# Performance work log

Measured on AMD Instinct MI355X. Metric: run time of the kernel, lower is better.

The kernel has to match this reference:

```python
import jax, jax.numpy as jnp
import numpy as np

N_NODES = 100000
N_EDGES = 1600000
D_FEAT = 128
NUM_UNITS = 128


def setup_inputs() -> dict:
    key = jax.random.key(0)
    k1, k2, k3, k4, k5 = jax.random.split(key, 5)
    H = jax.random.normal(k1, (N_NODES, D_FEAT), dtype=jnp.float32)
    edge_vals = jax.random.uniform(k2, (N_EDGES,), dtype=jnp.float32)
    W = jax.random.normal(k3, (D_FEAT, NUM_UNITS), dtype=jnp.float32) / np.sqrt(D_FEAT)
    b = jnp.zeros((NUM_UNITS,), dtype=jnp.float32)
    edge_src = jax.random.randint(k4, (N_EDGES,), 0, N_NODES, dtype=jnp.int32)
    edge_dst = jax.random.randint(k5, (N_EDGES,), 0, N_NODES, dtype=jnp.int32)
    return {"H": H, "edge_vals": edge_vals, "W": W, "b": b,
            "edge_src": edge_src, "edge_dst": edge_dst}


def reference(H, edge_vals, W, b, edge_src, edge_dst):
    # SpMM: AH[i] = sum_{e: src[e]==i} val[e] * H[dst[e]]
    gathered = edge_vals[:, None] * H[edge_dst]            # [E, F]
    AH = jax.ops.segment_sum(gathered, edge_src, num_segments=N_NODES)  # [N, F]
    # Dense projection + bias + relu (tf.layers.Dense with tf.nn.relu)
    return jax.nn.relu(AH @ W + b)
```

## Files before the change

kernel.cpp:

```cpp
#include <hip/hip_runtime.h>

#define N_NODES  100000
#define N_EDGES  1600000
#define D        128
#define NBUCK    1563
#define BCAP     1536
#define OCAP     8192
#define FCHUNK   8192

typedef __attribute__((ext_vector_type(8))) short bf16x8;
typedef __attribute__((ext_vector_type(4))) float f32x4;

__device__ __forceinline__ unsigned short f2bf(float x) {
    unsigned u = __float_as_uint(x);
    u += 0x7fffu + ((u >> 16) & 1u);
    return (unsigned short)(u >> 16);
}

__global__ __launch_bounds__(256) void wconvert(
    const float* __restrict__ W, unsigned short* __restrict__ Wfrag)
{
    int t = blockIdx.x * 256 + threadIdx.x;
    if (t >= 128 * 128) return;
    int k = t >> 7, n = t & 127;
    int c = n >> 4, cc = n & 15, ks = k >> 5, g = (k >> 3) & 3, j = k & 7;
    int lane = g * 16 + cc;
    Wfrag[(size_t)(((c * 4 + ks) * 64) + lane) * 8 + j] = f2bf(W[t]);
}

__global__ __launch_bounds__(256) void gemm_mfma(
    const float* __restrict__ H, const unsigned short* __restrict__ Wfrag,
    unsigned short* __restrict__ HWb)
{
    const int wid  = threadIdx.x >> 6;
    const int lane = threadIdx.x & 63;
    const int row16 = blockIdx.x * 64 + wid * 16;
    const int g = lane >> 4;

    int arow = row16 + (lane & 15);
    if (arow >= N_NODES) arow = N_NODES - 1;

    f32x4 acc[8];
#pragma unroll
    for (int c = 0; c < 8; ++c) acc[c] = (f32x4){0.f, 0.f, 0.f, 0.f};

#pragma unroll
    for (int ks = 0; ks < 4; ++ks) {
        const float* ap = H + (size_t)arow * D + ks * 32 + g * 8;
        float4 a0 = *reinterpret_cast<const float4*>(ap);
        float4 a1 = *reinterpret_cast<const float4*>(ap + 4);
        bf16x8 af;
        af[0] = (short)f2bf(a0.x); af[1] = (short)f2bf(a0.y);
        af[2] = (short)f2bf(a0.z); af[3] = (short)f2bf(a0.w);
        af[4] = (short)f2bf(a1.x); af[5] = (short)f2bf(a1.y);
        af[6] = (short)f2bf(a1.z); af[7] = (short)f2bf(a1.w);
#pragma unroll
        for (int c = 0; c < 8; ++c) {
            bf16x8 bf = *reinterpret_cast<const bf16x8*>(
                Wfrag + (size_t)((c * 4 + ks) * 64 + lane) * 8);
            acc[c] = __builtin_amdgcn_mfma_f32_16x16x32_bf16(af, bf, acc[c], 0, 0, 0);
        }
    }

#pragma unroll
    for (int c = 0; c < 8; ++c) {
#pragma unroll
        for (int r = 0; r < 4; ++r) {
            int orow = row16 + g * 4 + r;
            if (orow < N_NODES)
                HWb[(size_t)orow * D + c * 16 + (lane & 15)] = f2bf(acc[c][r]);
        }
    }
}

__global__ __launch_bounds__(256) void fill_bucket(
    const int* __restrict__ src, const int* __restrict__ dst,
    const float* __restrict__ vals, int* __restrict__ ccursor,
    int2* __restrict__ sedge_raw, int4* __restrict__ oflow,
    int* __restrict__ oflow_cnt)
{
    __shared__ int lhist[NBUCK];
    __shared__ int lbase[NBUCK];
    const int t = threadIdx.x;
    for (int i = t; i < NBUCK; i += 256) lhist[i] = 0;
    __syncthreads();
    const int e0 = blockIdx.x * FCHUNK;
    const int e1 = min(e0 + FCHUNK, N_EDGES);
    for (int e = e0 + t; e < e1; e += 256)
        atomicAdd(&lhist[src[e] >> 6], 1);
    __syncthreads();
    for (int i = t; i < NBUCK; i += 256) {
        int c = lhist[i];
        lbase[i] = c ? atomicAdd(&ccursor[i], c) : 0;
        lhist[i] = 0;
    }
    __syncthreads();
    for (int e = e0 + t; e < e1; e += 256) {
        int s = src[e];
        int bkt = s >> 6;
        int pos = lbase[bkt] + atomicAdd(&lhist[bkt], 1);
        if (pos < BCAP) {
            int2 p;
            p.x = dst[e] | ((s & 63) << 17);
            p.y = __float_as_int(vals[e]);
            sedge_raw[(size_t)bkt * BCAP + pos] = p;
        } else {
            int oc = atomicAdd(oflow_cnt, 1);
            if (oc < OCAP) oflow[oc] = make_int4(s, dst[e], __float_as_int(vals[e]), 0);
        }
    }
}

__global__ __launch_bounds__(256) void sort_gather(
    const unsigned short* __restrict__ HWb, const int2* __restrict__ sedge_raw,
    const int* __restrict__ ccursor, const int4* __restrict__ oflow,
    const int* __restrict__ oflow_cnt, const float* __restrict__ bias,
    float* __restrict__ out)
{
    __shared__ int2 eLds[BCAP];
    __shared__ int h[64];
    __shared__ int ex[64];
    __shared__ int cur[64];
    const int bkt = blockIdx.x;
    const int t = threadIdx.x;
    const size_t base = (size_t)bkt * BCAP;
    const int cnt = min(ccursor[bkt], BCAP);

    if (t < 64) h[t] = 0;
    __syncthreads();
    for (int j = t; j < cnt; j += 256)
        atomicAdd(&h[(sedge_raw[base + j].x >> 17) & 63], 1);
    __syncthreads();
    if (t < 64) {
        int v = h[t];
        int x = v;
        for (int off = 1; off < 64; off <<= 1) {
            int y = __shfl_up(x, off);
            if (t >= off) x += y;
        }
        ex[t] = x - v;
        cur[t] = 0;
    }
    __syncthreads();
    for (int j = t; j < cnt; j += 256) {
        int2 e = sedge_raw[base + j];
        int r = (e.x >> 17) & 63;
        int pos = ex[r] + atomicAdd(&cur[r], 1);
        e.x &= 0x1FFFF;
        eLds[pos] = e;
    }
    __syncthreads();

    const int wid = t >> 6, lane = t & 63;
    const int ovc = *oflow_cnt;
    const float2 bv = *reinterpret_cast<const float2*>(bias + lane * 2);
    for (int ln = wid; ln < 64; ln += 4) {
        int node = bkt * 64 + ln;
        if (node >= N_NODES) break;
        const int j0 = ex[ln], j1 = ex[ln] + h[ln];
        float ax = 0.f, ay = 0.f, bx = 0.f, by = 0.f;
        float cx = 0.f, cy = 0.f, dx = 0.f, dy = 0.f;
        int j = j0;
        for (; j + 4 <= j1; j += 4) {
            int2 e0 = eLds[j],     e1 = eLds[j + 1];
            int2 e2 = eLds[j + 2], e3 = eLds[j + 3];
            unsigned u0 = *reinterpret_cast<const unsigned*>(HWb + (size_t)e0.x * D + lane * 2);
            unsigned u1 = *reinterpret_cast<const unsigned*>(HWb + (size_t)e1.x * D + lane * 2);
            unsigned u2 = *reinterpret_cast<const unsigned*>(HWb + (size_t)e2.x * D + lane * 2);
            unsigned u3 = *reinterpret_cast<const unsigned*>(HWb + (size_t)e3.x * D + lane * 2);
            float v0 = __int_as_float(e0.y), v1 = __int_as_float(e1.y);
            float v2 = __int_as_float(e2.y), v3 = __int_as_float(e3.y);
            ax += v0 * __uint_as_float(u0 << 16);
            ay += v0 * __uint_as_float(u0 & 0xffff0000u);
            bx += v1 * __uint_as_float(u1 << 16);
            by += v1 * __uint_as_float(u1 & 0xffff0000u);
            cx += v2 * __uint_as_float(u2 << 16);
            cy += v2 * __uint_as_float(u2 & 0xffff0000u);
            dx += v3 * __uint_as_float(u3 << 16);
            dy += v3 * __uint_as_float(u3 & 0xffff0000u);
        }
        for (; j < j1; ++j) {
            int2 e = eLds[j];
            unsigned u = *reinterpret_cast<const unsigned*>(HWb + (size_t)e.x * D + lane * 2);
            float v = __int_as_float(e.y);
            ax += v * __uint_as_float(u << 16);
            ay += v * __uint_as_float(u & 0xffff0000u);
        }
        for (int q = 0; q < ovc; ++q) {
            int4 e = oflow[q];
            if (e.x == node) {
                unsigned u = *reinterpret_cast<const unsigned*>(HWb + (size_t)e.y * D + lane * 2);
                float v = __int_as_float(e.z);
                ax += v * __uint_as_float(u << 16);
                ay += v * __uint_as_float(u & 0xffff0000u);
            }
        }
        float2 o;
        o.x = fmaxf((ax + bx) + (cx + dx) + bv.x, 0.f);
        o.y = fmaxf((ay + by) + (cy + dy) + bv.y, 0.f);
        *reinterpret_cast<float2*>(out + (size_t)node * D + lane * 2) = o;
    }
}

extern "C" void kernel_launch(void* const* d_in, const int* in_sizes, int n_in,
                              void* d_out, int out_size, void* d_ws, size_t ws_size,
                              hipStream_t stream) {
    const float* H    = (const float*)d_in[0];
    const float* vals = (const float*)d_in[1];
    const float* W    = (const float*)d_in[2];
    const float* b    = (const float*)d_in[3];
    const int*   src  = (const int*)d_in[4];
    const int*   dst  = (const int*)d_in[5];
    float* out = (float*)d_out;

    unsigned short* HWb   = (unsigned short*)d_ws;
    unsigned short* Wfrag = HWb + (size_t)N_NODES * D;
    int2* sedge_raw = (int2*)(Wfrag + 128 * 128);
    int*  ccursor   = (int*)(sedge_raw + (size_t)NBUCK * BCAP);
    int*  oflow_cnt = ccursor + NBUCK;
    int4* oflow     = (int4*)(oflow_cnt + 3);

    hipMemsetAsync(ccursor, 0, (NBUCK + 1) * sizeof(int), stream);

    wconvert<<<64, 256, 0, stream>>>(W, Wfrag);
    gemm_mfma<<<(N_NODES + 63) / 64, 256, 0, stream>>>(H, Wfrag, HWb);
    fill_bucket<<<(N_EDGES + FCHUNK - 1) / FCHUNK, 256, 0, stream>>>(
        src, dst, vals, ccursor, sedge_raw, oflow, oflow_cnt);
    sort_gather<<<NBUCK, 256, 0, stream>>>(HWb, sedge_raw, ccursor, oflow,
                                           oflow_cnt, b, out);
}
```

Before: 134.2 us.

## Fuse weight convert, GEMM and edge bucketing into one launch; halve bucket size

Merges the W-conversion, MFMA projection and edge-bucket fill kernels into one heterogeneous launch. Blocks below GEMM_BLOCKS convert W into LDS and run the GEMM, and the remaining blocks bucket edges, so the two independent phases can run concurrently and two launches disappear. Buckets shrink from 64 to 32 nodes (3125 buckets, capacity 768), and sort_gather keeps its edges in registers instead of reading global memory twice. In exchange, every GEMM block re-reads and converts all of W, and the smaller buckets are more likely to overflow into the serial overflow list.

Measured after the change: 128.1 us. 1.05x faster.

```diff
diff --git a/kernel.cpp b/kernel.cpp
--- a/kernel.cpp
+++ b/kernel.cpp
@@ -3,10 +3,11 @@
 #define N_NODES  100000
 #define N_EDGES  1600000
 #define D        128
-#define NBUCK    1563
-#define BCAP     1536
+#define NBUCK    3125
+#define BCAP     768
 #define OCAP     8192
-#define FCHUNK   8192
+#define FCHUNK   4096
+#define GEMM_BLOCKS 1563
 
 typedef __attribute__((ext_vector_type(8))) short bf16x8;
 typedef __attribute__((ext_vector_type(4))) float f32x4;
@@ -17,96 +18,110 @@
     return (unsigned short)(u >> 16);
 }
 
-__global__ __launch_bounds__(256) void wconvert(
-    const float* __restrict__ W, unsigned short* __restrict__ Wfrag)
+__global__ __launch_bounds__(256) void mega(
+    const float* __restrict__ H, const float* __restrict__ W,
+    const int* __restrict__ src, const int* __restrict__ dst,
+    const float* __restrict__ vals, unsigned short* __restrict__ HWb,
+    int* __restrict__ ccursor, int2* __restrict__ sedge_raw,
+    int4* __restrict__ oflow, int* __restrict__ oflow_cnt)
 {
-    int t = blockIdx.x * 256 + threadIdx.x;
-    if (t >= 128 * 128) return;
-    int k = t >> 7, n = t & 127;
-    int c = n >> 4, cc = n & 15, ks = k >> 5, g = (k >> 3) & 3, j = k & 7;
-    int lane = g * 16 + cc;
-    Wfrag[(size_t)(((c * 4 + ks) * 64) + lane) * 8 + j] = f2bf(W[t]);
-}
-
-__global__ __launch_bounds__(256) void gemm_mfma(
-    const float* __restrict__ H, const unsigned short* __restrict__ Wfrag,
-    unsigned short* __restrict__ HWb)
-{
-    const int wid  = threadIdx.x >> 6;
-    const int lane = threadIdx.x & 63;
-    const int row16 = blockIdx.x * 64 + wid * 16;
-    const int g = lane >> 4;
-
-    int arow = row16 + (lane & 15);
-    if (arow >= N_NODES) arow = N_NODES - 1;
-
-    f32x4 acc[8];
-#pragma unroll
-    for (int c = 0; c < 8; ++c) acc[c] = (f32x4){0.f, 0.f, 0.f, 0.f};
-
-#pragma unroll
-    for (int ks = 0; ks < 4; ++ks) {
-        const float* ap = H + (size_t)arow * D + ks * 32 + g * 8;
-        float4 a0 = *reinterpret_cast<const float4*>(ap);
-        float4 a1 = *reinterpret_cast<const float4*>(ap + 4);
-        bf16x8 af;
-        af[0] = (short)f2bf(a0.x); af[1] = (short)f2bf(a0.y);
-        af[2] = (short)f2bf(a0.z); af[3] = (short)f2bf(a0.w);
-        af[4] = (short)f2bf(a1.x); af[5] = (short)f2bf(a1.y);
-        af[6] = (short)f2bf(a1.z); af[7] = (short)f2bf(a1.w);
+    __shared__ char smem[32768];
+    const int t = threadIdx.x;
+
+    if (blockIdx.x < GEMM_BLOCKS) {
+        short* wlds = (short*)smem;
+        {
+            const int n   = t & 127;
+            const int kb0 = (t >> 7) * 4;
+            const int c = n >> 4, cc = n & 15;
+#pragma unroll
+            for (int q = 0; q < 16; ++q) {
+                int kbase = q * 8 + kb0;
+                float w0 = W[(kbase + 0) * 128 + n];
+                float w1 = W[(kbase + 1) * 128 + n];
+                float w2 = W[(kbase + 2) * 128 + n];
+                float w3 = W[(kbase + 3) * 128 + n];
+                int ks = kbase >> 5, g = (kbase >> 3) & 3, j0 = kbase & 7;
+                short4 pk;
+                pk.x = (short)f2bf(w0);
+                pk.y = (short)f2bf(w1);
+                pk.z = (short)f2bf(w2);
+                pk.w = (short)f2bf(w3);
+                *reinterpret_cast<short4*>(
+                    &wlds[(size_t)(((c * 4 + ks) * 64) + g * 16 + cc) * 8 + j0]) = pk;
+            }
+        }
+        __syncthreads();
+
+        const int wid  = t >> 6;
+        const int lane = t & 63;
+        const int row16 = blockIdx.x * 64 + wid * 16;
+        const int g = lane >> 4;
+
+        int arow = row16 + (lane & 15);
+        if (arow >= N_NODES) arow = N_NODES - 1;
+
+        f32x4 acc[8];
+#pragma unroll
+        for (int c = 0; c < 8; ++c) acc[c] = (f32x4){0.f, 0.f, 0.f, 0.f};
+
+#pragma unroll
+        for (int ks = 0; ks < 4; ++ks) {
+            const float* ap = H + (size_t)arow * D + ks * 32 + g * 8;
+            float4 a0 = *reinterpret_cast<const float4*>(ap);
+            float4 a1 = *reinterpret_cast<const float4*>(ap + 4);
+            bf16x8 af;
+            af[0] = (short)f2bf(a0.x); af[1] = (short)f2bf(a0.y);
+            af[2] = (short)f2bf(a0.z); af[3] = (short)f2bf(a0.w);
+            af[4] = (short)f2bf(a1.x); af[5] = (short)f2bf(a1.y);
+            af[6] = (short)f2bf(a1.z); af[7] = (short)f2bf(a1.w);
+#pragma unroll
+            for (int c = 0; c < 8; ++c) {
+                bf16x8 bf = *reinterpret_cast<const bf16x8*>(
+                    &wlds[(size_t)((c * 4 + ks) * 64 + lane) * 8]);
+                acc[c] = __builtin_amdgcn_mfma_f32_16x16x32_bf16(af, bf, acc[c], 0, 0, 0);
+            }
+        }
+
 #pragma unroll
         for (int c = 0; c < 8; ++c) {
-            bf16x8 bf = *reinterpret_cast<const bf16x8*>(
-                Wfrag + (size_t)((c * 4 + ks) * 64 + lane) * 8);
-            acc[c] = __builtin_amdgcn_mfma_f32_16x16x32_bf16(af, bf, acc[c], 0, 0, 0);
-        }
-    }
-
-#pragma unroll
-    for (int c = 0; c < 8; ++c) {
-#pragma unroll
-        for (int r = 0; r < 4; ++r) {
-            int orow = row16 + g * 4 + r;
-            if (orow < N_NODES)
-                HWb[(size_t)orow * D + c * 16 + (lane & 15)] = f2bf(acc[c][r]);
-        }
-    }
-}
-
-__global__ __launch_bounds__(256) void fill_bucket(
-    const int* __restrict__ src, const int* __restrict__ dst,
-    const float* __restrict__ vals, int* __restrict__ ccursor,
-    int2* __restrict__ sedge_raw, int4* __restrict__ oflow,
-    int* __restrict__ oflow_cnt)
-{
-    __shared__ int lhist[NBUCK];
-    __shared__ int lbase[NBUCK];
-    const int t = threadIdx.x;
-    for (int i = t; i < NBUCK; i += 256) lhist[i] = 0;
-    __syncthreads();
-    const int e0 = blockIdx.x * FCHUNK;
-    const int e1 = min(e0 + FCHUNK, N_EDGES);
-    for (int e = e0 + t; e < e1; e += 256)
-        atomicAdd(&lhist[src[e] >> 6], 1);
-    __syncthreads();
-    for (int i = t; i < NBUCK; i += 256) {
-        int c = lhist[i];
-        lbase[i] = c ? atomicAdd(&ccursor[i], c) : 0;
-        lhist[i] = 0;
-    }
-    __syncthreads();
-    for (int e = e0 + t; e < e1; e += 256) {
-        int s = src[e];
-        int bkt = s >> 6;
-        int pos = lbase[bkt] + atomicAdd(&lhist[bkt], 1);
-        if (pos < BCAP) {
-            int2 p;
-            p.x = dst[e] | ((s & 63) << 17);
-            p.y = __float_as_int(vals[e]);
-            sedge_raw[(size_t)bkt * BCAP + pos] = p;
-        } else {
-            int oc = atomicAdd(oflow_cnt, 1);
-            if (oc < OCAP) oflow[oc] = make_int4(s, dst[e], __float_as_int(vals[e]), 0);
+#pragma unroll
+            for (int r = 0; r < 4; ++r) {
+                int orow = row16 + g * 4 + r;
+                if (orow < N_NODES)
+                    HWb[(size_t)orow * D + c * 16 + (lane & 15)] = f2bf(acc[c][r]);
+            }
+        }
+    } else {
+        int* lhist = (int*)smem;
+        int* lbase = lhist + NBUCK;
+        for (int i = t; i < NBUCK; i += 256) lhist[i] = 0;
+        __syncthreads();
+        const int fb = blockIdx.x - GEMM_BLOCKS;
+        const int e0 = fb * FCHUNK;
+        const int e1 = min(e0 + FCHUNK, N_EDGES);
+        for (int e = e0 + t; e < e1; e += 256)
+            atomicAdd(&lhist[src[e] >> 5], 1);
+        __syncthreads();
+        for (int i = t; i < NBUCK; i += 256) {
+            int c = lhist[i];
+            lbase[i] = c ? atomicAdd(&ccursor[i], c) : 0;
+            lhist[i] = 0;
+        }
+        __syncthreads();
+        for (int e = e0 + t; e < e1; e += 256) {
+            int s = src[e];
+            int bkt = s >> 5;
+            int pos = lbase[bkt] + atomicAdd(&lhist[bkt], 1);
+            if (pos < BCAP) {
+                int2 p;
+                p.x = dst[e] | ((s & 31) << 17);
+                p.y = __float_as_int(vals[e]);
+                sedge_raw[(size_t)bkt * BCAP + pos] = p;
+            } else {
+                int oc = atomicAdd(oflow_cnt, 1);
+                if (oc < OCAP) oflow[oc] = make_int4(s, dst[e], __float_as_int(vals[e]), 0);
+            }
         }
     }
 }
@@ -118,23 +133,33 @@
     float* __restrict__ out)
 {
     __shared__ int2 eLds[BCAP];
-    __shared__ int h[64];
-    __shared__ int ex[64];
-    __shared__ int cur[64];
+    __shared__ int h[32];
+    __shared__ int ex[32];
+    __shared__ int cur[32];
     const int bkt = blockIdx.x;
     const int t = threadIdx.x;
     const size_t base = (size_t)bkt * BCAP;
     const int cnt = min(ccursor[bkt], BCAP);
 
-    if (t < 64) h[t] = 0;
-    __syncthreads();
-    for (int j = t; j < cnt; j += 256)
-        atomicAdd(&h[(sedge_raw[base + j].x >> 17) & 63], 1);
-    __syncthreads();
-    if (t < 64) {
+    if (t < 32) { h[t] = 0; }
+    __syncthreads();
+
+    int2 myE[3]; int myR[3];
+#pragma unroll
+    for (int q = 0; q < 3; ++q) {
+        int j = t + q * 256;
+        myR[q] = -1;
+        if (j < cnt) {
+            myE[q] = sedge_raw[base + j];
+            myR[q] = (myE[q].x >> 17) & 31;
+            atomicAdd(&h[myR[q]], 1);
+        }
+    }
+    __syncthreads();
+    if (t < 32) {
         int v = h[t];
         int x = v;
-        for (int off = 1; off < 64; off <<= 1) {
+        for (int off = 1; off < 32; off <<= 1) {
             int y = __shfl_up(x, off);
             if (t >= off) x += y;
         }
@@ -142,21 +167,23 @@
         cur[t] = 0;
     }
     __syncthreads();
-    for (int j = t; j < cnt; j += 256) {
-        int2 e = sedge_raw[base + j];
-        int r = (e.x >> 17) & 63;
-        int pos = ex[r] + atomicAdd(&cur[r], 1);
-        e.x &= 0x1FFFF;
-        eLds[pos] = e;
+#pragma unroll
+    for (int q = 0; q < 3; ++q) {
+        if (myR[q] >= 0) {
+            int pos = ex[myR[q]] + atomicAdd(&cur[myR[q]], 1);
+            int2 e;
+            e.x = myE[q].x & 0x1FFFF;
+            e.y = myE[q].y;
+            eLds[pos] = e;
+        }
     }
     __syncthreads();
 
     const int wid = t >> 6, lane = t & 63;
     const int ovc = *oflow_cnt;
     const float2 bv = *reinterpret_cast<const float2*>(bias + lane * 2);
-    for (int ln = wid; ln < 64; ln += 4) {
-        int node = bkt * 64 + ln;
-        if (node >= N_NODES) break;
+    for (int ln = wid; ln < 32; ln += 4) {
+        int node = bkt * 32 + ln;
         const int j0 = ex[ln], j1 = ex[ln] + h[ln];
         float ax = 0.f, ay = 0.f, bx = 0.f, by = 0.f;
         float cx = 0.f, cy = 0.f, dx = 0.f, dy = 0.f;
@@ -213,19 +240,17 @@
     const int*   dst  = (const int*)d_in[5];
     float* out = (float*)d_out;
 
-    unsigned short* HWb   = (unsigned short*)d_ws;
-    unsigned short* Wfrag = HWb + (size_t)N_NODES * D;
-    int2* sedge_raw = (int2*)(Wfrag + 128 * 128);
+    unsigned short* HWb = (unsigned short*)d_ws;
+    int2* sedge_raw = (int2*)(HWb + (size_t)N_NODES * D);
     int*  ccursor   = (int*)(sedge_raw + (size_t)NBUCK * BCAP);
     int*  oflow_cnt = ccursor + NBUCK;
     int4* oflow     = (int4*)(oflow_cnt + 3);
 
     hipMemsetAsync(ccursor, 0, (NBUCK + 1) * sizeof(int), stream);
 
-    wconvert<<<64, 256, 0, stream>>>(W, Wfrag);
-    gemm_mfma<<<(N_NODES + 63) / 64, 256, 0, stream>>>(H, Wfrag, HWb);
-    fill_bucket<<<(N_EDGES + FCHUNK - 1) / FCHUNK, 256, 0, stream>>>(
-        src, dst, vals, ccursor, sedge_raw, oflow, oflow_cnt);
+    const int FILL_BLOCKS = (N_EDGES + FCHUNK - 1) / FCHUNK;
+    mega<<<GEMM_BLOCKS + FILL_BLOCKS, 256, 0, stream>>>(
+        H, W, src, dst, vals, HWb, ccursor, sedge_raw, oflow, oflow_cnt);
     sort_gather<<<NBUCK, 256, 0, stream>>>(HWb, sedge_raw, ccursor, oflow,
                                            oflow_cnt, b, out);
 }
```
